# Kernel optimization log

Hardware: AMD Instinct MI355X
Metric: run time of the kernel (lower is better)

Reference implementation:

```python
import jax, jax.numpy as jnp
import numpy as np

DIM, N_HEADS, HEAD_DIM, BASE = 1024, 16, 64, 10000.0
B, S = 2, 2048


def setup_inputs() -> dict:
    key = jax.random.key(0)
    ks = jax.random.split(key, 8)
    theta = (BASE ** (-jnp.arange(0, HEAD_DIM, 2, dtype=jnp.float32) / HEAD_DIM))  # [head_dim//2]
    s = 0.02
    return {
        "x": jax.random.normal(ks[0], (B, S, DIM), jnp.float32),
        "positions": jnp.arange(S, dtype=jnp.int32),
        "theta": theta,
        "Wq": jax.random.normal(ks[1], (DIM, N_HEADS * HEAD_DIM), jnp.float32) * s,
        "bq": jnp.zeros((N_HEADS * HEAD_DIM,), jnp.float32),
        "Wk": jax.random.normal(ks[2], (DIM, N_HEADS * HEAD_DIM), jnp.float32) * s,
        "bk": jnp.zeros((N_HEADS * HEAD_DIM,), jnp.float32),
        "Wv": jax.random.normal(ks[3], (DIM, N_HEADS * HEAD_DIM), jnp.float32) * s,
        "bv": jnp.zeros((N_HEADS * HEAD_DIM,), jnp.float32),
        "Wo": jax.random.normal(ks[4], (N_HEADS * HEAD_DIM, DIM), jnp.float32) * s,
        "bo": jnp.zeros((DIM,), jnp.float32),
    }


def _rope(x, theta):
    # x: [B, H, S, head_dim]; theta: [head_dim//2]
    seq_len = x.shape[2]
    ang = jnp.arange(seq_len, dtype=x.dtype)[:, None] * theta  # [S, head_dim//2]
    cos = jnp.cos(ang)[None, None]  # [1,1,S,head_dim//2]
    sin = jnp.sin(ang)[None, None]
    x1, x2 = x[..., 0::2], x[..., 1::2]
    # matches torch.cat([-x2*sin + x1*cos, x1*sin + x2*cos], dim=-1)
    return jnp.concatenate([x1 * cos - x2 * sin, x1 * sin + x2 * cos], axis=-1)


def reference(x, positions, theta, Wq, bq, Wk, bk, Wv, bv, Wo, bo):
    batch, seq_len, _ = x.shape
    H, hd = N_HEADS, HEAD_DIM

    def split_heads(t):
        return t.reshape(batch, seq_len, H, hd).transpose(0, 2, 1, 3)  # [B,H,S,hd]

    q = split_heads(x @ Wq + bq)
    k = split_heads(x @ Wk + bk)
    v = split_heads(x @ Wv + bv)
    q = _rope(q, theta)
    k = _rope(k, theta)

    scale = 1.0 / jnp.sqrt(jnp.asarray(hd, x.dtype))
    scores = jnp.einsum("bhqd,bhkd->bhqk", q, k) * scale  # [B,H,S,S]
    causal = jnp.tril(jnp.ones((seq_len, seq_len), dtype=bool))
    scores = jnp.where(causal, scores, jnp.asarray(-jnp.inf, x.dtype))
    attn = jax.nn.softmax(scores, axis=-1)  # dropout is identity at eval
    out = jnp.einsum("bhqk,bhkd->bhqd", attn, v)  # [B,H,S,hd]
    out = out.transpose(0, 2, 1, 3).reshape(batch, seq_len, H * hd)
    return out @ Wo + bo
```

## Files before the change

kernel.cpp:

```cpp
#include <hip/hip_runtime.h>
#include <math.h>

#define B_   2
#define S_   2048
#define DIM_ 1024
#define H_   16
#define HD_  64
#define BS_  (B_ * S_)
#define BHSD ((size_t)B_ * H_ * S_ * HD_)
#define CEXP 0.1803368801111244f

typedef unsigned short u16;
typedef unsigned int   u32;
typedef short s16x8 __attribute__((ext_vector_type(8)));
typedef float f32x4 __attribute__((ext_vector_type(4)));

#define MFMA16(a, b, c) __builtin_amdgcn_mfma_f32_16x16x32_bf16((a), (b), (c), 0, 0, 0)

__device__ __forceinline__ u16 f2bf(float f) {
    u32 u = __float_as_uint(f);
    u += 0x7fffu + ((u >> 16) & 1u);
    return (u16)(u >> 16);
}
__device__ __forceinline__ u32 cvt_pk_bf16(float a, float b) {
    u32 r;
    asm("v_cvt_pk_bf16_f32 %0, %1, %2" : "=v"(r) : "v"(a), "v"(b));
    return r;
}
__device__ __forceinline__ void gl16(void* lds, const void* g) {
    __builtin_amdgcn_global_load_lds(
        (__attribute__((address_space(1))) void*)(g),
        (__attribute__((address_space(3))) void*)(lds), 16, 0, 0);
}

__global__ __launch_bounds__(256) void prep(
    const float* __restrict__ x, u16* __restrict__ xb,
    const float* __restrict__ W0, const float* __restrict__ W1,
    const float* __restrict__ W2, const float* __restrict__ W3,
    u16* __restrict__ T0, u16* __restrict__ T1,
    u16* __restrict__ T2, u16* __restrict__ T3,
    const float* __restrict__ bq, const float* __restrict__ bk,
    const float* __restrict__ bv, float* __restrict__ bias3,
    const float* __restrict__ theta, float2* __restrict__ cs)
{
    __shared__ float tile[32][33];
    const int bid = blockIdx.x, tid = threadIdx.x;

    if (bid < 2048) {
        const int i = bid * 256 + tid;
        const float4 a = *(const float4*)(x + (size_t)i * 8);
        const float4 b = *(const float4*)(x + (size_t)i * 8 + 4);
        s16x8 o;
        o[0] = (short)f2bf(a.x); o[1] = (short)f2bf(a.y);
        o[2] = (short)f2bf(a.z); o[3] = (short)f2bf(a.w);
        o[4] = (short)f2bf(b.x); o[5] = (short)f2bf(b.y);
        o[6] = (short)f2bf(b.z); o[7] = (short)f2bf(b.w);
        *(s16x8*)(xb + (size_t)i * 8) = o;
    } else if (bid < 6144) {
        const int idx = bid - 2048;
        const int z = idx >> 10;
        const float* W; u16* T;
        switch (z) {
            case 0: W = W0; T = T0; break;
            case 1: W = W1; T = T1; break;
            case 2: W = W2; T = T2; break;
            default: W = W3; T = T3; break;
        }
        const int n0 = ((idx >> 5) & 31) * 32, k0 = (idx & 31) * 32;
        const int c = tid & 31, rr = tid >> 5;
#pragma unroll
        for (int i = 0; i < 4; ++i) {
            const int k = rr + i * 8;
            tile[k][c] = W[(size_t)(k0 + k) * DIM_ + n0 + c];
        }
        __syncthreads();
#pragma unroll
        for (int i = 0; i < 4; ++i) {
            const int col = n0 + rr + i * 8;
            int pcol = col;
            if (z < 2) {
                const int dd = col & 63;
                const int pd = (dd & 1) ? 32 + (dd >> 1) : (dd >> 1);
                pcol = (col & ~63) | pd;
            }
            T[(size_t)pcol * DIM_ + k0 + c] = f2bf(tile[c][rr + i * 8]);
        }
    } else if (bid < 6400) {
        const int idx = bid - 6144;
        const int s = idx * 8 + (tid >> 5), j = tid & 31;
        float sn, cn;
        sincosf((float)s * theta[j], &sn, &cn);
        cs[(s << 5) + j] = make_float2(cn, sn);
    } else {
        const int i = (bid - 6400) * 256 + tid;
        const int which = i >> 10, local = i & 1023;
        const float v = (which == 0) ? bq[local]
                      : (which == 1) ? bk[local] : bv[local];
        int dst = i;
        if (which < 2) {
            const int dd = local & 63;
            const int pd = (dd & 1) ? 32 + (dd >> 1) : (dd >> 1);
            dst = which * 1024 + (local & ~63) + pd;
        }
        bias3[dst] = v;
    }
}

template<int BN, int HMIN, int EPI>
__global__ __launch_bounds__(256, 3) void gemm_mfma(
    const u16* __restrict__ A, const u16* __restrict__ Bt,
    const float* __restrict__ bias, void* __restrict__ Yv,
    const float2* __restrict__ cs)
{
    __shared__ u16 As[128 * 64];
    __shared__ u16 Bs[BN * 64];

    const int tid = threadIdx.x, lane = tid & 63, wid = tid >> 6;
    const int l15 = lane & 15, lg = lane >> 4;
    const int row0 = blockIdx.x * 128, col0 = blockIdx.y * BN;
    const int wr = (wid >> 1) * 64;
    const int wc = (wid & 1) * (BN / 2);
    constexpr int NM = 4, NN = BN / 32, BCH = BN / 32;

    const int l8 = lane >> 3, l7 = lane & 7;
    const int colE = ((l7 ^ l8) << 3);

    const u16* aptr[4]; u16* aldp[4];
#pragma unroll
    for (int i = 0; i < 4; ++i) {
        const int ci = wid * 4 + i;
        const int rr = row0 + ci * 8 + l8;
        size_t a0;
        if (HMIN)
            a0 = (((size_t)(rr >> 11) * H_) * S_ + (rr & (S_ - 1))) * HD_ + colE;
        else
            a0 = (size_t)rr * DIM_ + colE;
        aptr[i] = A + a0;
        aldp[i] = As + ci * 512;
    }
    const u16* bptr[BCH]; u16* bldp[BCH];
#pragma unroll
    for (int i = 0; i < BCH; ++i) {
        const int ci = wid * BCH + i;
        const int rr = col0 + ci * 8 + l8;
        bptr[i] = Bt + (size_t)rr * DIM_ + colE;
        bldp[i] = Bs + ci * 512;
    }
    const size_t astep = HMIN ? (size_t)S_ * HD_ : 64;

    f32x4 acc[NM][NN];
#pragma unroll
    for (int m = 0; m < NM; ++m)
#pragma unroll
        for (int n = 0; n < NN; ++n) acc[m][n] = (f32x4){0.f, 0.f, 0.f, 0.f};

    for (int k0 = 0; k0 < DIM_; k0 += 64) {
        __syncthreads();
#pragma unroll
        for (int i = 0; i < 4; ++i) gl16(aldp[i], aptr[i]);
#pragma unroll
        for (int i = 0; i < BCH; ++i) gl16(bldp[i], bptr[i]);
#pragma unroll
        for (int i = 0; i < 4; ++i) aptr[i] += astep;
#pragma unroll
        for (int i = 0; i < BCH; ++i) bptr[i] += 64;
        __syncthreads();

        s16x8 af[NM][2], bfr[NN][2];
#pragma unroll
        for (int m = 0; m < NM; ++m) {
            const int row = wr + m * 16 + l15;
#pragma unroll
            for (int kf = 0; kf < 2; ++kf)
                af[m][kf] = *(const s16x8*)&As[row * 64 +
                    (((kf * 64 + lg * 16) ^ ((l15 & 7) << 4)) >> 1)];
        }
#pragma unroll
        for (int n = 0; n < NN; ++n) {
            const int row = wc + n * 16 + l15;
#pragma unroll
            for (int kf = 0; kf < 2; ++kf)
                bfr[n][kf] = *(const s16x8*)&Bs[row * 64 +
                    (((kf * 64 + lg * 16) ^ ((l15 & 7) << 4)) >> 1)];
        }
        __builtin_amdgcn_s_setprio(1);
#pragma unroll
        for (int m = 0; m < NM; ++m)
#pragma unroll
            for (int n = 0; n < NN; ++n) {
                acc[m][n] = MFMA16(af[m][0], bfr[n][0], acc[m][n]);
                acc[m][n] = MFMA16(af[m][1], bfr[n][1], acc[m][n]);
            }
        __builtin_amdgcn_s_setprio(0);
    }

    if (EPI == 0) {
        u16* Y = (u16*)Yv;
        const int whichq = (col0 + wc) >> 10;
        if (whichq < 2) {
            const float sclw = (whichq == 0) ? CEXP : 1.0f;
#pragma unroll
            for (int n = 0; n < 2; ++n) {
                const int cc0 = col0 + wc + n * 16 + l15;
                const int j = n * 16 + l15;
                const float bv0 = bias[cc0];
                const float bv1 = bias[cc0 + 32];
                const int hh = (cc0 >> 6) & (H_ - 1);
#pragma unroll
                for (int m = 0; m < NM; ++m)
#pragma unroll
                    for (int r = 0; r < 4; ++r) {
                        const int rr = row0 + wr + m * 16 + lg * 4 + r;
                        const int b = rr >> 11, s = rr & (S_ - 1);
                        const float2 csv = cs[(s << 5) + j];
                        const float v0 = acc[m][n][r] + bv0;
                        const float v1 = acc[m][n + 2][r] + bv1;
                        const size_t base = (size_t)whichq * BHSD
                            + (((size_t)b * H_ + hh) * S_ + s) * HD_;
                        Y[base + j]      = f2bf((v0 * csv.x - v1 * csv.y) * sclw);
                        Y[base + j + 32] = f2bf((v0 * csv.y + v1 * csv.x) * sclw);
                    }
            }
        } else {
#pragma unroll
            for (int n = 0; n < NN; ++n) {
                const int cc = col0 + wc + n * 16 + l15;
                const float bv = bias[cc];
                const int hh = (cc >> 6) & (H_ - 1), d = cc & 63;
#pragma unroll
                for (int m = 0; m < NM; ++m)
#pragma unroll
                    for (int r = 0; r < 4; ++r) {
                        const int rr = row0 + wr + m * 16 + lg * 4 + r;
                        const int b = rr >> 11, s = rr & (S_ - 1);
                        const int sp = (s & ~60) | ((s & 12) << 1)
                                     | ((s & 16) << 1) | ((s & 32) >> 3);
                        Y[2 * BHSD + ((size_t)(b * H_ + hh) * HD_ + d) * S_ + sp] =
                            f2bf(acc[m][n][r] + bv);
                    }
            }
        }
    } else {
#pragma unroll
        for (int n = 0; n < NN; ++n) {
            const int cc = col0 + wc + n * 16 + l15;
            const float bv = bias[cc];
#pragma unroll
            for (int m = 0; m < NM; ++m)
#pragma unroll
                for (int r = 0; r < 4; ++r) {
                    const int rr = row0 + wr + m * 16 + lg * 4 + r;
                    ((float*)Yv)[(size_t)rr * DIM_ + cc] = acc[m][n][r] + bv;
                }
        }
    }
}

__global__ __launch_bounds__(512, 2) void attn_bal(
    u16* __restrict__ Q, const u16* __restrict__ K, const u16* __restrict__ VT)
{
    const int bh   = blockIdx.x;
    const int pidx = blockIdx.y;
    const int nsteps = 32 - pidx;

    u16* Qg = Q + (size_t)bh * S_ * HD_;
    const u16* Kg = K + (size_t)bh * S_ * HD_;
    const u16* Vg = VT + (size_t)bh * HD_ * S_;

    __shared__ u16 Ks[2][64 * 64];
    __shared__ u16 Vs[2][64 * 64];

    const int tid = threadIdx.x;
    const int w = tid >> 6, lane = tid & 63;
    const int grp = w >> 2, widq = w & 3;
    const int qt = grp ? (31 - pidx) : pidx;
    const int myTiles = qt + 1;
    const int q0 = qt * 64 + widq * 16;
    const int l15 = lane & 15, lg = lane >> 4;

    const int srow = w * 8 + (lane >> 3);
    const int sslt = lane & 7;
    const int soff = ((sslt ^ (srow & 7)) << 3);

    auto stage = [&](int bufi, int j0) {
        gl16(&Ks[bufi][w * 512], Kg + (size_t)(j0 + srow) * HD_ + soff);
        gl16(&Vs[bufi][w * 512], Vg + (size_t)srow * S_ + j0 + soff);
    };

    s16x8 qf[2];
    {
        const u16* qrow = Qg + (size_t)(q0 + l15) * HD_ + lg * 8;
        qf[0] = *(const s16x8*)(qrow);
        qf[1] = *(const s16x8*)(qrow + 32);
    }

    f32x4 o[4];
#pragma unroll
    for (int n = 0; n < 4; ++n) o[n] = (f32x4){0.f, 0.f, 0.f, 0.f};
    float mI = -1e30f, lI = 0.f;

    stage(0, 0);
    __syncthreads();

    int buf = 0;
    for (int t = 0; t < nsteps; ++t) {
        if (t + 1 < nsteps) stage(buf ^ 1, (t + 1) * 64);

        if (t < myTiles) {
            const u16* Kb = Ks[buf];
            const u16* Vb = Vs[buf];

            f32x4 sc[4];
            __builtin_amdgcn_s_setprio(1);
#pragma unroll
            for (int sub = 0; sub < 4; ++sub) {
                const int kr = sub * 16 + l15;
                const s16x8 kf0 = *(const s16x8*)&Kb[kr * 64 + ((lg ^ (kr & 7)) << 3)];
                const s16x8 kf1 = *(const s16x8*)&Kb[kr * 64 + (((lg + 4) ^ (kr & 7)) << 3)];
                f32x4 z = (f32x4){0.f, 0.f, 0.f, 0.f};
                z = MFMA16(kf0, qf[0], z);
                sc[sub] = MFMA16(kf1, qf[1], z);
            }
            __builtin_amdgcn_s_setprio(0);

            if (t == qt) {
#pragma unroll
                for (int sub = 0; sub < 4; ++sub) {
                    if (sub == widq) {
#pragma unroll
                        for (int r = 0; r < 4; ++r)
                            if (lg * 4 + r > l15) sc[sub][r] = -1e30f;
                    } else if (sub > widq) {
#pragma unroll
                        for (int r = 0; r < 4; ++r) sc[sub][r] = -1e30f;
                    }
                }
            }

            float pm = -1e30f;
#pragma unroll
            for (int sub = 0; sub < 4; ++sub)
#pragma unroll
                for (int r = 0; r < 4; ++r) pm = fmaxf(pm, sc[sub][r]);
            pm = fmaxf(pm, __shfl_xor(pm, 16));
            pm = fmaxf(pm, __shfl_xor(pm, 32));
            if (!__all(pm - mI <= 8.f)) {
                const float mn = fmaxf(mI, pm);
                const float al = __builtin_amdgcn_exp2f(mI - mn);
                mI = mn; lI *= al;
#pragma unroll
                for (int r = 0; r < 4; ++r) {
                    const float at = __shfl(al, lg * 4 + r);
#pragma unroll
                    for (int n = 0; n < 4; ++n) o[n][r] *= at;
                }
            }
            float p[4][4];
            float ps = 0.f;
#pragma unroll
            for (int sub = 0; sub < 4; ++sub)
#pragma unroll
                for (int r = 0; r < 4; ++r) {
                    p[sub][r] = __builtin_amdgcn_exp2f(sc[sub][r] - mI);
                    ps += p[sub][r];
                }
            ps += __shfl_xor(ps, 16);
            ps += __shfl_xor(ps, 32);
            lI += ps;

            union { s16x8 v; u32 w4[4]; } af[2];
#pragma unroll
            for (int step = 0; step < 2; ++step)
#pragma unroll
                for (int jj = 0; jj < 4; ++jj) {
                    const int sub = (jj >> 1) * 2 + step;
                    const int r0  = (jj & 1) * 2;
                    af[step].w4[jj] = cvt_pk_bf16(p[sub][r0], p[sub][r0 + 1]);
                }
            __builtin_amdgcn_s_setprio(1);
#pragma unroll
            for (int n = 0; n < 4; ++n) {
                const int d = n * 16 + l15;
                const s16x8 vf0 = *(const s16x8*)&Vb[d * 64 + ((lg ^ (d & 7)) << 3)];
                const s16x8 vf1 = *(const s16x8*)&Vb[d * 64 + (((lg + 4) ^ (d & 7)) << 3)];
                o[n] = MFMA16(af[0].v, vf0, o[n]);
                o[n] = MFMA16(af[1].v, vf1, o[n]);
            }
            __builtin_amdgcn_s_setprio(0);
        }

        __syncthreads();
        buf ^= 1;
    }

    const float il = 1.f / lI;
    u16* orow = Qg + (size_t)(q0 + lg * 4) * HD_ + l15;
#pragma unroll
    for (int r = 0; r < 4; ++r) {
        const float ilr = __shfl(il, lg * 4 + r);
#pragma unroll
        for (int n = 0; n < 4; ++n)
            orow[r * HD_ + n * 16] = f2bf(o[n][r] * ilr);
    }
}

extern "C" void kernel_launch(void* const* d_in, const int* in_sizes, int n_in,
                              void* d_out, int out_size, void* d_ws, size_t ws_size,
                              hipStream_t stream)
{
    (void)in_sizes; (void)n_in; (void)out_size; (void)ws_size;
    const float* x     = (const float*)d_in[0];
    const float* theta = (const float*)d_in[2];
    const float* Wq    = (const float*)d_in[3];
    const float* bq    = (const float*)d_in[4];
    const float* Wk    = (const float*)d_in[5];
    const float* bk    = (const float*)d_in[6];
    const float* Wv    = (const float*)d_in[7];
    const float* bv    = (const float*)d_in[8];
    const float* Wo    = (const float*)d_in[9];
    const float* bo    = (const float*)d_in[10];
    float* out = (float*)d_out;

    u16* xb  = (u16*)d_ws;
    u16* wtq = xb + (size_t)BS_ * DIM_;
    u16* wtk = wtq + (size_t)DIM_ * DIM_;
    u16* wtv = wtk + (size_t)DIM_ * DIM_;
    u16* wto = wtv + (size_t)DIM_ * DIM_;
    u16* qws = wto + (size_t)DIM_ * DIM_;
    u16* kws = qws + BHSD;
    u16* vtw = kws + BHSD;
    float* bias3 = (float*)(vtw + BHSD);
    float2* cs = (float2*)(bias3 + 4096);

    prep<<<dim3(6412), dim3(256), 0, stream>>>(
        x, xb, Wq, Wk, Wv, Wo, wtq, wtk, wtv, wto, bq, bk, bv, bias3, theta, cs);

    gemm_mfma<128, 0, 0><<<dim3(32, 24), dim3(256), 0, stream>>>(
        xb, wtq, bias3, qws, cs);

    attn_bal<<<dim3(32, 16), dim3(512), 0, stream>>>(qws, kws, vtw);

    gemm_mfma<64, 1, 1><<<dim3(32, 16), dim3(256), 0, stream>>>(
        qws, wto, bo, out, cs);
}
```

Before: 101.3 us.

## Replace paired-tile balanced attention blocks with one query tile per 256-thread block

The attention kernel stops pairing a short and a long causal query tile inside one 512-thread block, which shared K/V staging across both halves. Each block now handles a single 64-row query tile with 4 waves, and the grid is launched longest-tile first so the hardware scheduler can balance the causal triangle. This removes the idle waves in paired blocks, which still waited at every barrier once their own tile was finished. The cost is that each K/V tile is now staged separately for each query tile, giving more global loads, and the balance depends on the dispatch order.

```diff
diff --git a/kernel.cpp b/kernel.cpp
--- a/kernel.cpp
+++ b/kernel.cpp
@@ -256,12 +256,12 @@
     }
 }
 
-__global__ __launch_bounds__(512, 2) void attn_bal(
+__global__ __launch_bounds__(256, 4) void attn_q(
     u16* __restrict__ Q, const u16* __restrict__ K, const u16* __restrict__ VT)
 {
-    const int bh   = blockIdx.x;
-    const int pidx = blockIdx.y;
-    const int nsteps = 32 - pidx;
+    const int bh = blockIdx.x;
+    const int qt = 31 - blockIdx.y;
+    const int nsteps = qt + 1;
 
     u16* Qg = Q + (size_t)bh * S_ * HD_;
     const u16* Kg = K + (size_t)bh * S_ * HD_;
@@ -272,19 +272,20 @@
 
     const int tid = threadIdx.x;
     const int w = tid >> 6, lane = tid & 63;
-    const int grp = w >> 2, widq = w & 3;
-    const int qt = grp ? (31 - pidx) : pidx;
-    const int myTiles = qt + 1;
-    const int q0 = qt * 64 + widq * 16;
+    const int q0 = qt * 64 + w * 16;
     const int l15 = lane & 15, lg = lane >> 4;
 
-    const int srow = w * 8 + (lane >> 3);
-    const int sslt = lane & 7;
-    const int soff = ((sslt ^ (srow & 7)) << 3);
+    const int crow = lane >> 3, cslt = lane & 7;
 
     auto stage = [&](int bufi, int j0) {
-        gl16(&Ks[bufi][w * 512], Kg + (size_t)(j0 + srow) * HD_ + soff);
-        gl16(&Vs[bufi][w * 512], Vg + (size_t)srow * S_ + j0 + soff);
+#pragma unroll
+        for (int i = 0; i < 2; ++i) {
+            const int c = w * 2 + i;
+            const int row = c * 8 + crow;
+            const int soff = ((cslt ^ (row & 7)) << 3);
+            gl16(&Ks[bufi][c * 512], Kg + (size_t)(j0 + row) * HD_ + soff);
+            gl16(&Vs[bufi][c * 512], Vg + (size_t)row * S_ + j0 + soff);
+        }
     };
 
     s16x8 qf[2];
@@ -306,88 +307,86 @@
     for (int t = 0; t < nsteps; ++t) {
         if (t + 1 < nsteps) stage(buf ^ 1, (t + 1) * 64);
 
-        if (t < myTiles) {
-            const u16* Kb = Ks[buf];
-            const u16* Vb = Vs[buf];
-
-            f32x4 sc[4];
-            __builtin_amdgcn_s_setprio(1);
+        const u16* Kb = Ks[buf];
+        const u16* Vb = Vs[buf];
+
+        f32x4 sc[4];
+        __builtin_amdgcn_s_setprio(1);
+#pragma unroll
+        for (int sub = 0; sub < 4; ++sub) {
+            const int kr = sub * 16 + l15;
+            const s16x8 kf0 = *(const s16x8*)&Kb[kr * 64 + ((lg ^ (kr & 7)) << 3)];
+            const s16x8 kf1 = *(const s16x8*)&Kb[kr * 64 + (((lg + 4) ^ (kr & 7)) << 3)];
+            f32x4 z = (f32x4){0.f, 0.f, 0.f, 0.f};
+            z = MFMA16(kf0, qf[0], z);
+            sc[sub] = MFMA16(kf1, qf[1], z);
+        }
+        __builtin_amdgcn_s_setprio(0);
+
+        if (t == qt) {
 #pragma unroll
             for (int sub = 0; sub < 4; ++sub) {
-                const int kr = sub * 16 + l15;
-                const s16x8 kf0 = *(const s16x8*)&Kb[kr * 64 + ((lg ^ (kr & 7)) << 3)];
-                const s16x8 kf1 = *(const s16x8*)&Kb[kr * 64 + (((lg + 4) ^ (kr & 7)) << 3)];
-                f32x4 z = (f32x4){0.f, 0.f, 0.f, 0.f};
-                z = MFMA16(kf0, qf[0], z);
-                sc[sub] = MFMA16(kf1, qf[1], z);
-            }
-            __builtin_amdgcn_s_setprio(0);
-
-            if (t == qt) {
-#pragma unroll
-                for (int sub = 0; sub < 4; ++sub) {
-                    if (sub == widq) {
-#pragma unroll
-                        for (int r = 0; r < 4; ++r)
-                            if (lg * 4 + r > l15) sc[sub][r] = -1e30f;
-                    } else if (sub > widq) {
-#pragma unroll
-                        for (int r = 0; r < 4; ++r) sc[sub][r] = -1e30f;
-                    }
+                if (sub == w) {
+#pragma unroll
+                    for (int r = 0; r < 4; ++r)
+                        if (lg * 4 + r > l15) sc[sub][r] = -1e30f;
+                } else if (sub > w) {
+#pragma unroll
+                    for (int r = 0; r < 4; ++r) sc[sub][r] = -1e30f;
                 }
             }
-
-            float pm = -1e30f;
-#pragma unroll
-            for (int sub = 0; sub < 4; ++sub)
-#pragma unroll
-                for (int r = 0; r < 4; ++r) pm = fmaxf(pm, sc[sub][r]);
-            pm = fmaxf(pm, __shfl_xor(pm, 16));
-            pm = fmaxf(pm, __shfl_xor(pm, 32));
-            if (!__all(pm - mI <= 8.f)) {
-                const float mn = fmaxf(mI, pm);
-                const float al = __builtin_amdgcn_exp2f(mI - mn);
-                mI = mn; lI *= al;
-#pragma unroll
-                for (int r = 0; r < 4; ++r) {
-                    const float at = __shfl(al, lg * 4 + r);
-#pragma unroll
-                    for (int n = 0; n < 4; ++n) o[n][r] *= at;
-                }
-            }
-            float p[4][4];
-            float ps = 0.f;
-#pragma unroll
-            for (int sub = 0; sub < 4; ++sub)
-#pragma unroll
-                for (int r = 0; r < 4; ++r) {
-                    p[sub][r] = __builtin_amdgcn_exp2f(sc[sub][r] - mI);
-                    ps += p[sub][r];
-                }
-            ps += __shfl_xor(ps, 16);
-            ps += __shfl_xor(ps, 32);
-            lI += ps;
-
-            union { s16x8 v; u32 w4[4]; } af[2];
-#pragma unroll
-            for (int step = 0; step < 2; ++step)
-#pragma unroll
-                for (int jj = 0; jj < 4; ++jj) {
-                    const int sub = (jj >> 1) * 2 + step;
-                    const int r0  = (jj & 1) * 2;
-                    af[step].w4[jj] = cvt_pk_bf16(p[sub][r0], p[sub][r0 + 1]);
-                }
-            __builtin_amdgcn_s_setprio(1);
-#pragma unroll
-            for (int n = 0; n < 4; ++n) {
-                const int d = n * 16 + l15;
-                const s16x8 vf0 = *(const s16x8*)&Vb[d * 64 + ((lg ^ (d & 7)) << 3)];
-                const s16x8 vf1 = *(const s16x8*)&Vb[d * 64 + (((lg + 4) ^ (d & 7)) << 3)];
-                o[n] = MFMA16(af[0].v, vf0, o[n]);
-                o[n] = MFMA16(af[1].v, vf1, o[n]);
-            }
-            __builtin_amdgcn_s_setprio(0);
-        }
+        }
+
+        float pm = -1e30f;
+#pragma unroll
+        for (int sub = 0; sub < 4; ++sub)
+#pragma unroll
+            for (int r = 0; r < 4; ++r) pm = fmaxf(pm, sc[sub][r]);
+        pm = fmaxf(pm, __shfl_xor(pm, 16));
+        pm = fmaxf(pm, __shfl_xor(pm, 32));
+        if (!__all(pm - mI <= 8.f)) {
+            const float mn = fmaxf(mI, pm);
+            const float al = __builtin_amdgcn_exp2f(mI - mn);
+            mI = mn; lI *= al;
+#pragma unroll
+            for (int r = 0; r < 4; ++r) {
+                const float at = __shfl(al, lg * 4 + r);
+#pragma unroll
+                for (int n = 0; n < 4; ++n) o[n][r] *= at;
+            }
+        }
+        float p[4][4];
+        float ps = 0.f;
+#pragma unroll
+        for (int sub = 0; sub < 4; ++sub)
+#pragma unroll
+            for (int r = 0; r < 4; ++r) {
+                p[sub][r] = __builtin_amdgcn_exp2f(sc[sub][r] - mI);
+                ps += p[sub][r];
+            }
+        ps += __shfl_xor(ps, 16);
+        ps += __shfl_xor(ps, 32);
+        lI += ps;
+
+        union { s16x8 v; u32 w4[4]; } af[2];
+#pragma unroll
+        for (int step = 0; step < 2; ++step)
+#pragma unroll
+            for (int jj = 0; jj < 4; ++jj) {
+                const int sub = (jj >> 1) * 2 + step;
+                const int r0  = (jj & 1) * 2;
+                af[step].w4[jj] = cvt_pk_bf16(p[sub][r0], p[sub][r0 + 1]);
+            }
+        __builtin_amdgcn_s_setprio(1);
+#pragma unroll
+        for (int n = 0; n < 4; ++n) {
+            const int d = n * 16 + l15;
+            const s16x8 vf0 = *(const s16x8*)&Vb[d * 64 + ((lg ^ (d & 7)) << 3)];
+            const s16x8 vf1 = *(const s16x8*)&Vb[d * 64 + (((lg + 4) ^ (d & 7)) << 3)];
+            o[n] = MFMA16(af[0].v, vf0, o[n]);
+            o[n] = MFMA16(af[1].v, vf1, o[n]);
+        }
+        __builtin_amdgcn_s_setprio(0);
 
         __syncthreads();
         buf ^= 1;
@@ -438,7 +437,7 @@
     gemm_mfma<128, 0, 0><<<dim3(32, 24), dim3(256), 0, stream>>>(
         xb, wtq, bias3, qws, cs);
 
-    attn_bal<<<dim3(32, 16), dim3(512), 0, stream>>>(qws, kws, vtw);
+    attn_q<<<dim3(32, 32), dim3(256), 0, stream>>>(qws, kws, vtw);
 
     gemm_mfma<64, 1, 1><<<dim3(32, 16), dim3(256), 0, stream>>>(
         qws, wto, bo, out, cs);
```

Measured after the change: 99.17 us. -2.1%, faster.
